# Kernel optimization log

Hardware: AMD Instinct MI355X
Metric: run time of the kernel (lower is better)

## Reference

```python
import jax, jax.numpy as jnp
import numpy as np

N, E = 50000, 800000
NFEAT, NHID, NHEADS, NCLASS = 512, 64, 8, 64
ALPHA = 0.2  # leaky relu negative slope


def setup_inputs() -> dict:
    key = jax.random.key(0)
    ks = jax.random.split(key, 8)
    x = jax.random.normal(ks[0], (N, NFEAT), jnp.float32)
    row = jax.random.randint(ks[1], (E,), 0, N)  # destination node i of each edge
    col = jax.random.randint(ks[2], (E,), 0, N)  # source node j of each edge
    W = jax.random.normal(ks[3], (NHEADS, NFEAT, NHID), jnp.float32) * (1.0 / np.sqrt(NFEAT))
    a = jax.random.normal(ks[4], (NHEADS, 2 * NHID), jnp.float32) * 0.1
    W_out = jax.random.normal(ks[5], (NHID * NHEADS, NCLASS), jnp.float32) * (1.0 / np.sqrt(NHID * NHEADS))
    a_out = jax.random.normal(ks[6], (2 * NCLASS,), jnp.float32) * 0.1
    return {"x": x, "row": row, "col": col, "W": W, "a": a, "W_out": W_out, "a_out": a_out}


def _gat_layer(h, W, a, row, col, n, alpha, concat):
    # h: [N, F_in], W: [F_in, F'], a: [2*F']
    Wh = h @ W                                   # [N, F']
    f = Wh.shape[-1]
    f_dst = Wh @ a[:f]                           # a^T part for target node i, [N]
    f_src = Wh @ a[f:]                           # a^T part for source node j, [N]
    e = jax.nn.leaky_relu(f_dst[row] + f_src[col], alpha)       # [E] attention logits
    # numerically stable segment softmax over incoming edges of each node
    m = jax.ops.segment_max(e, row, num_segments=n)
    m = jnp.where(jnp.isneginf(m), 0.0, m)       # nodes with no in-edges
    p = jnp.exp(e - m[row])
    denom = jax.ops.segment_sum(p, row, num_segments=n)
    att = p / jnp.maximum(denom[row], 1e-16)     # [E]
    out = jax.ops.segment_sum(att[:, None] * Wh[col], row, num_segments=n)  # [N, F']
    return jax.nn.elu(out) if concat else out


def reference(x, row, col, W, a, W_out, a_out):
    # eval mode: F.dropout is a no-op
    heads = [_gat_layer(x, W[h], a[h], row, col, N, ALPHA, True) for h in range(NHEADS)]
    h = jnp.concatenate(heads, axis=1)           # [N, NHID*NHEADS]
    return _gat_layer(h, W_out, a_out, row, col, N, ALPHA, False)  # [N, NCLASS]
```

## Files before the change

### kernel.cpp

```cpp
#include <hip/hip_runtime.h>
#include <cstdint>
#include <cstddef>

#define NN      50000
#define MPAD    50048
#define EE      800000
#define NHEADS  8
#define HID_TOT 512
#define NCLASS  64
#define ALPHA_LRELU 0.2f
#define NB1     196
#define CAP1    128
#define CAP2    128

typedef unsigned short u16;
typedef __attribute__((ext_vector_type(8))) unsigned short ushort8;
typedef __attribute__((ext_vector_type(4))) unsigned short ushort4v;

__device__ __forceinline__ float bf2f(u16 v) {
    return __uint_as_float(((unsigned)v) << 16);
}
__device__ __forceinline__ u16 f2bf(float f) {
    unsigned u = __float_as_uint(f);
    return (u16)((u + 0x7fffu + ((u >> 16) & 1u)) >> 16);
}

#define PREP_R0 (MPAD * 64)
#define PREP_R1 (512 * 512)
#define PREP_R2 (64 * 512)
#define PREP_R3 ((MPAD - NN) * 64)
#define PREP_TOT (PREP_R0 + PREP_R1 + PREP_R2 + PREP_R3)

__global__ __launch_bounds__(256) void prep_all(const float* __restrict__ x,
                                                const float* __restrict__ W,
                                                const float* __restrict__ W_out,
                                                u16* __restrict__ xb,
                                                u16* __restrict__ Wt1,
                                                u16* __restrict__ Wto,
                                                u16* __restrict__ h1b) {
    int g = blockIdx.x * 256 + threadIdx.x;
    if (g < PREP_R0) {
        int r = g >> 6;
        int c = (g & 63) * 8;
        ushort8 o = (ushort8)0;
        if (r < NN) {
            const float4 v0 = *(const float4*)(x + (size_t)r * 512 + c);
            const float4 v1 = *(const float4*)(x + (size_t)r * 512 + c + 4);
            o[0] = f2bf(v0.x); o[1] = f2bf(v0.y); o[2] = f2bf(v0.z); o[3] = f2bf(v0.w);
            o[4] = f2bf(v1.x); o[5] = f2bf(v1.y); o[6] = f2bf(v1.z); o[7] = f2bf(v1.w);
        }
        *(ushort8*)(xb + (size_t)r * 512 + c) = o;
        return;
    }
    g -= PREP_R0;
    if (g < PREP_R1) {
        int c = g >> 9, f = g & 511;
        int h = c >> 6, j = c & 63;
        Wt1[g] = f2bf(W[(h << 15) + (f << 6) + j]);
        return;
    }
    g -= PREP_R1;
    if (g < PREP_R2) {
        int n = g >> 9, k = g & 511;
        Wto[g] = f2bf(W_out[k * 64 + n]);
        return;
    }
    g -= PREP_R2;
    if (g < PREP_R3) {
        *(ushort8*)(h1b + (size_t)NN * 512 + (size_t)g * 8) = (ushort8)0;
    }
}


__global__ void fill_i32(int* __restrict__ p, int v, long n) {
    long i = (long)blockIdx.x * blockDim.x + threadIdx.x;
    if (i < n) p[i] = v;
}

__global__ void hist_rows(const int* __restrict__ row, int* __restrict__ cnt) {
    int e = blockIdx.x * 256 + threadIdx.x;
    if (e >= EE) return;
    atomicAdd(&cnt[row[e]], 1);
}

__global__ __launch_bounds__(256) void scan_blocksum(const int* __restrict__ cnt,
                                                     int* __restrict__ bsum) {
    int idx = blockIdx.x * 256 + threadIdx.x;
    int v = (idx < NN) ? cnt[idx] : 0;
    #pragma unroll
    for (int o = 32; o; o >>= 1) v += __shfl_xor(v, o);
    __shared__ int sw[4];
    int wave = threadIdx.x >> 6;
    if ((threadIdx.x & 63) == 0) sw[wave] = v;
    __syncthreads();
    if (threadIdx.x == 0) bsum[blockIdx.x] = sw[0] + sw[1] + sw[2] + sw[3];
}

__global__ __launch_bounds__(256) void scan_bsums(const int* __restrict__ bsum,
                                                  int* __restrict__ boff) {
    __shared__ int sh[256];
    int t = threadIdx.x;
    int v = (t < NB1) ? bsum[t] : 0;
    sh[t] = v;
    __syncthreads();
    for (int o = 1; o < 256; o <<= 1) {
        int cur = sh[t];
        int add = (t >= o) ? sh[t - o] : 0;
        __syncthreads();
        sh[t] = cur + add;
        __syncthreads();
    }
    if (t < NB1) boff[t] = sh[t] - v;
}

__global__ __launch_bounds__(256) void scan_write(const int* __restrict__ cnt,
                                                  const int* __restrict__ boff,
                                                  int* __restrict__ start,
                                                  int* __restrict__ wr) {
    __shared__ int sh[256];
    int t = threadIdx.x;
    int idx = blockIdx.x * 256 + t;
    int c = (idx < NN) ? cnt[idx] : 0;
    sh[t] = c;
    __syncthreads();
    for (int o = 1; o < 256; o <<= 1) {
        int cur = sh[t];
        int add = (t >= o) ? sh[t - o] : 0;
        __syncthreads();
        sh[t] = cur + add;
        __syncthreads();
    }
    if (idx < NN) {
        int excl = boff[blockIdx.x] + sh[t] - c;
        start[idx] = excl;
        wr[idx] = excl;
    }
    if (idx == 0) start[NN] = EE;
}

__global__ void scatter_edges(const int* __restrict__ row, const int* __restrict__ col,
                              int* __restrict__ wr, int* __restrict__ ecol) {
    int e = blockIdx.x * 256 + threadIdx.x;
    if (e >= EE) return;
    int i = row[e];
    int pos = atomicAdd(&wr[i], 1);
    ecol[pos] = col[e];
}


__device__ __forceinline__ void load_lds_128(const u16* g, u16* l) {
    __builtin_amdgcn_global_load_lds((const __attribute__((address_space(1))) void*)g,
                                     (__attribute__((address_space(3))) void*)l,
                                     16, 0, 0);
}

typedef __attribute__((ext_vector_type(8))) short frag8;
typedef __attribute__((ext_vector_type(4))) float f32x4;

template <int BN, int OUT_MODE, bool FUSE_DOTS>
__global__ __launch_bounds__(256) void gemm_bf16(const u16* __restrict__ A,
                                                 const u16* __restrict__ Bt,
                                                 void* __restrict__ Cv,
                                                 int M, int N, int K,
                                                 const float* __restrict__ av,
                                                 float* __restrict__ fd,
                                                 float* __restrict__ fs) {
    constexpr int BM = 128, BK = 32;
    constexpr int WN = BN / 2;
    constexpr int NT = WN / 16;
    __shared__ u16 As[BM * BK];
    __shared__ u16 Bs[BN * BK];
    const int tid = threadIdx.x;
    const int wave = tid >> 6, lane = tid & 63;
    const int wm = wave & 1, wn = wave >> 1;
    const int bm = blockIdx.y * BM, bn = blockIdx.x * BN;
    const int q = lane >> 4, lr = lane & 15;

    f32x4 acc[4][NT] = {};

    for (int k0 = 0; k0 < K; k0 += BK) {
        #pragma unroll
        for (int c = wave; c < (BM * BK) / 512; c += 4) {
            int f = c * 512 + lane * 8;
            int row = f >> 5, ck = f & 31;
            load_lds_128(A + (size_t)(bm + row) * K + k0 + ck, As + c * 512);
        }
        #pragma unroll
        for (int c = wave; c < (BN * BK) / 512; c += 4) {
            int f = c * 512 + lane * 8;
            int row = f >> 5, ck = f & 31;
            load_lds_128(Bt + (size_t)(bn + row) * K + k0 + ck, Bs + c * 512);
        }
        __syncthreads();
        frag8 af[4], bfr[NT];
        #pragma unroll
        for (int am = 0; am < 4; am++)
            af[am] = *(const frag8*)(As + (wm * 64 + am * 16 + lr) * 32 + q * 8);
        #pragma unroll
        for (int bt = 0; bt < NT; bt++)
            bfr[bt] = *(const frag8*)(Bs + (wn * WN + bt * 16 + lr) * 32 + q * 8);
        #pragma unroll
        for (int am = 0; am < 4; am++)
            #pragma unroll
            for (int bt = 0; bt < NT; bt++)
                acc[am][bt] = __builtin_amdgcn_mfma_f32_16x16x32_bf16(af[am], bfr[bt], acc[am][bt], 0, 0, 0);
        __syncthreads();
    }

    float adv[NT], adv2[NT];
    int hd = 0;
    if (FUSE_DOTS) {
        hd = blockIdx.x * 2 + wn;
        const float* ah = av + hd * 128;
        #pragma unroll
        for (int bt = 0; bt < NT; bt++) {
            adv[bt]  = ah[bt * 16 + lr];
            adv2[bt] = ah[64 + bt * 16 + lr];
        }
    }

    #pragma unroll
    for (int am = 0; am < 4; am++) {
        #pragma unroll
        for (int reg = 0; reg < 4; reg++) {
            int gr = bm + wm * 64 + am * 16 + q * 4 + reg;
            bool inb = gr < M;
            if (inb) {
                #pragma unroll
                for (int bt = 0; bt < NT; bt++) {
                    int gc = bn + wn * WN + bt * 16 + lr;
                    float v = acc[am][bt][reg];
                    if (OUT_MODE == 0) ((float*)Cv)[(size_t)gr * N + gc] = v;
                    else               ((u16*)Cv)[(size_t)gr * N + gc] = f2bf(v);
                }
            }
            if (FUSE_DOTS) {
                float sd = 0.f, ss = 0.f;
                #pragma unroll
                for (int bt = 0; bt < NT; bt++) {
                    float v = acc[am][bt][reg];
                    sd += v * adv[bt];
                    ss += v * adv2[bt];
                }
                #pragma unroll
                for (int o = 1; o < 16; o <<= 1) {
                    sd += __shfl_xor(sd, o);
                    ss += __shfl_xor(ss, o);
                }
                if (lr == 0 && inb) {
                    fd[gr * 8 + hd] = sd;
                    fs[gr * 8 + hd] = ss;
                }
            }
        }
    }
}


__global__ __launch_bounds__(256) void dots2(const u16* __restrict__ Wh2b, const float* __restrict__ a_out,
                                             float* __restrict__ fd, float* __restrict__ fs) {
    __shared__ float as[128];
    if (threadIdx.x < 128) as[threadIdx.x] = a_out[threadIdx.x];
    __syncthreads();
    int n = blockIdx.x * 256 + threadIdx.x;
    if (n >= NN) return;
    const u16* w = Wh2b + (size_t)n * NCLASS;
    float sd = 0.f, ss = 0.f;
    #pragma unroll
    for (int c = 0; c < 8; c++) {
        ushort8 v8 = *(const ushort8*)(w + c * 8);
        #pragma unroll
        for (int k = 0; k < 8; k++) {
            float v = bf2f(v8[k]);
            sd += v * as[c * 8 + k];
            ss += v * as[64 + c * 8 + k];
        }
    }
    fd[n] = sd;
    fs[n] = ss;
}

__global__ __launch_bounds__(256) void agg1_fused(const int* __restrict__ start,
                                                  const int* __restrict__ ecol,
                                                  const float* __restrict__ fd,
                                                  const float* __restrict__ fs,
                                                  const u16* __restrict__ Whb,
                                                  u16* __restrict__ h1b) {
    __shared__ float vc[4][CAP1 * 8];
    const int w = threadIdx.x >> 6;
    const int i = blockIdx.x * 4 + w;
    const int lane = threadIdx.x & 63;
    const int g = lane >> 3, h = lane & 7;
    const int st = start[i], en = start[i + 1];

    const float fdv1 = fd[i * 8 + h];
    float m = -__builtin_huge_valf();
    for (int t = st + g; t < en; t += 8) {
        int j = ecol[t];
        float v = fdv1 + fs[j * 8 + h];
        v = v > 0.f ? v : ALPHA_LRELU * v;
        int c = t - st;
        if (c < CAP1) vc[w][c * 8 + h] = v;
        m = fmaxf(m, v);
    }
    m = fmaxf(m, __shfl_xor(m, 8));
    m = fmaxf(m, __shfl_xor(m, 16));
    m = fmaxf(m, __shfl_xor(m, 32));
    __syncthreads();

    const int hh = lane >> 3;
    const float mh = __shfl(m, hh);
    const float fdv2 = fd[i * 8 + hh];
    float acc[8] = {};
    float den = 0.f;
    int t = st;
    for (; t + 2 <= en; t += 2) {
        int c0 = t - st, c1 = c0 + 1;
        int j0 = ecol[t], j1 = ecol[t + 1];
        float v0, v1;
        if (c1 < CAP1) {
            v0 = vc[w][c0 * 8 + hh];
            v1 = vc[w][c1 * 8 + hh];
        } else {
            v0 = fdv2 + fs[j0 * 8 + hh]; v0 = v0 > 0.f ? v0 : ALPHA_LRELU * v0;
            v1 = fdv2 + fs[j1 * 8 + hh]; v1 = v1 > 0.f ? v1 : ALPHA_LRELU * v1;
        }
        float p0 = __expf(v0 - mh);
        float p1 = __expf(v1 - mh);
        den += p0 + p1;
        ushort8 w0 = *(const ushort8*)(Whb + (size_t)j0 * HID_TOT + lane * 8);
        ushort8 w1 = *(const ushort8*)(Whb + (size_t)j1 * HID_TOT + lane * 8);
        #pragma unroll
        for (int k = 0; k < 8; k++) acc[k] += p0 * bf2f(w0[k]);
        #pragma unroll
        for (int k = 0; k < 8; k++) acc[k] += p1 * bf2f(w1[k]);
    }
    if (t < en) {
        int c = t - st;
        int j = ecol[t];
        float v;
        if (c < CAP1) v = vc[w][c * 8 + hh];
        else { v = fdv2 + fs[j * 8 + hh]; v = v > 0.f ? v : ALPHA_LRELU * v; }
        float p = __expf(v - mh);
        den += p;
        ushort8 wv = *(const ushort8*)(Whb + (size_t)j * HID_TOT + lane * 8);
        #pragma unroll
        for (int k = 0; k < 8; k++) acc[k] += p * bf2f(wv[k]);
    }
    float rden = 1.0f / fmaxf(den, 1e-16f);
    ushort8 o8;
    #pragma unroll
    for (int k = 0; k < 8; k++) {
        float v = acc[k] * rden;
        v = v > 0.f ? v : (__expf(v) - 1.0f);
        o8[k] = f2bf(v);
    }
    *(ushort8*)(h1b + (size_t)i * HID_TOT + lane * 8) = o8;
}

__global__ __launch_bounds__(256) void agg2_fused(const int* __restrict__ start,
                                                  const int* __restrict__ ecol,
                                                  const float* __restrict__ fd,
                                                  const float* __restrict__ fs,
                                                  const u16* __restrict__ Wh2b,
                                                  float* __restrict__ out) {
    __shared__ float vc[4][CAP2];
    const int w = threadIdx.x >> 6;
    const int i = blockIdx.x * 4 + w;
    const int lane = threadIdx.x & 63;
    const int st = start[i], en = start[i + 1];
    const float fdv = fd[i];

    float m = -__builtin_huge_valf();
    for (int t = st + lane; t < en; t += 64) {
        int j = ecol[t];
        float v = fdv + fs[j];
        v = v > 0.f ? v : ALPHA_LRELU * v;
        int c = t - st;
        if (c < CAP2) vc[w][c] = v;
        m = fmaxf(m, v);
    }
    #pragma unroll
    for (int o = 32; o; o >>= 1) m = fmaxf(m, __shfl_xor(m, o));
    __syncthreads();

    const int g = lane >> 4, r = lane & 15;
    float acc[4] = {};
    float den = 0.f;
    for (int t = st + g; t < en; t += 4) {
        int c = t - st;
        float v;
        if (c < CAP2) {
            v = vc[w][c];
        } else {
            int jj = ecol[t];
            v = fdv + fs[jj];
            v = v > 0.f ? v : ALPHA_LRELU * v;
        }
        float p = __expf(v - m);
        den += p;
        int j = ecol[t];
        ushort4v wv = *(const ushort4v*)(Wh2b + (size_t)j * NCLASS + r * 4);
        #pragma unroll
        for (int k = 0; k < 4; k++) acc[k] += p * bf2f(wv[k]);
    }
    #pragma unroll
    for (int o = 16; o <= 32; o <<= 1) {
        den += __shfl_xor(den, o);
        #pragma unroll
        for (int k = 0; k < 4; k++) acc[k] += __shfl_xor(acc[k], o);
    }
    if (g == 0) {
        float rden = 1.0f / fmaxf(den, 1e-16f);
        float4 o4;
        o4.x = acc[0] * rden; o4.y = acc[1] * rden;
        o4.z = acc[2] * rden; o4.w = acc[3] * rden;
        *(float4*)(out + (size_t)i * NCLASS + r * 4) = o4;
    }
}


static inline int cdiv_l(long a, long b) { return (int)((a + b - 1) / b); }

extern "C" void kernel_launch(void* const* d_in, const int* in_sizes, int n_in,
                              void* d_out, int out_size, void* d_ws, size_t ws_size,
                              hipStream_t stream) {
    const float* x     = (const float*)d_in[0];
    const int*   row   = (const int*)d_in[1];
    const int*   col   = (const int*)d_in[2];
    const float* W     = (const float*)d_in[3];
    const float* a     = (const float*)d_in[4];
    const float* W_out = (const float*)d_in[5];
    const float* a_out = (const float*)d_in[6];
    float* out = (float*)d_out;

    char* wsb = (char*)d_ws;
    size_t off = 0;
    auto alloc = [&](size_t bytes) { char* p = wsb + off; off += (bytes + 255) & ~(size_t)255; return p; };
    u16*   xb     = (u16*)  alloc((size_t)MPAD * 512 * 2);
    u16*   Wcat_t = (u16*)  alloc((size_t)512 * 512 * 2);
    u16*   Wot_t  = (u16*)  alloc((size_t)64 * 512 * 2);
    u16*   Whb1   = (u16*)  alloc((size_t)NN * 512 * 2);
    float* fd1    = (float*)alloc((size_t)NN * 8 * 4);
    float* fs1    = (float*)alloc((size_t)NN * 8 * 4);
    u16*   h1b    = (u16*)  alloc((size_t)MPAD * 512 * 2);
    u16*   Wh2b   = (u16*)  alloc((size_t)NN * 64 * 2);
    float* fd2    = (float*)alloc((size_t)NN * 4);
    float* fs2    = (float*)alloc((size_t)NN * 4);
    int*   cnt    = (int*)  alloc((size_t)NN * 4);
    int*   startp = (int*)  alloc(((size_t)NN + 1) * 4);
    int*   wr     = (int*)  alloc((size_t)NN * 4);
    int*   ecol   = (int*)  alloc((size_t)EE * 4);
    int*   bsum   = (int*)  alloc((size_t)NB1 * 4);
    int*   boff   = (int*)  alloc((size_t)NB1 * 4);

    fill_i32<<<cdiv_l(NN, 256), 256, 0, stream>>>(cnt, 0, (long)NN);
    hist_rows<<<cdiv_l(EE, 256), 256, 0, stream>>>(row, cnt);
    scan_blocksum<<<NB1, 256, 0, stream>>>(cnt, bsum);
    scan_bsums<<<1, 256, 0, stream>>>(bsum, boff);
    scan_write<<<NB1, 256, 0, stream>>>(cnt, boff, startp, wr);
    scatter_edges<<<cdiv_l(EE, 256), 256, 0, stream>>>(row, col, wr, ecol);

    prep_all<<<cdiv_l(PREP_TOT, 256), 256, 0, stream>>>(x, W, W_out, xb, Wcat_t, Wot_t, h1b);

    {
        dim3 grid(512 / 128, cdiv_l(MPAD, 128));
        gemm_bf16<128, 1, true><<<grid, 256, 0, stream>>>(xb, Wcat_t, Whb1, NN, 512, 512,
                                                          a, fd1, fs1);
    }
    agg1_fused<<<NN / 4, 256, 0, stream>>>(startp, ecol, fd1, fs1, Whb1, h1b);

    {
        dim3 grid(1, cdiv_l(MPAD, 128));
        gemm_bf16<64, 1, false><<<grid, 256, 0, stream>>>(h1b, Wot_t, Wh2b, NN, 64, 512,
                                                          nullptr, nullptr, nullptr);
    }
    dots2<<<cdiv_l(NN, 256), 256, 0, stream>>>(Wh2b, a_out, fd2, fs2);
    agg2_fused<<<NN / 4, 256, 0, stream>>>(startp, ecol, fd2, fs2, Wh2b, out);
}
```

Baseline: 493.3 us.

## Drop softmax max pass, fuse second-layer attention dots into GEMM epilogue

Both aggregation kernels now compute exp(logit) directly, without the per-node max-reduction pass and its LDS cache of logits. This removes a full extra sweep over each node's edges and the associated gathers. The separate dots2 kernel is folded into the second GEMM's epilogue via a shared-memory partial reduction across waves. The zeroing of the padded h1b rows is also dropped. Skipping the max shift risks overflow in exp for large logits, and the padded rows are now left uninitialised.

```diff
diff --git a/kernel.cpp b/kernel.cpp
--- a/kernel.cpp
+++ b/kernel.cpp
@@ -10,8 +10,6 @@
 #define NCLASS  64
 #define ALPHA_LRELU 0.2f
 #define NB1     196
-#define CAP1    128
-#define CAP2    128
 
 typedef unsigned short u16;
 typedef __attribute__((ext_vector_type(8))) unsigned short ushort8;
@@ -28,16 +26,14 @@
 #define PREP_R0 (MPAD * 64)
 #define PREP_R1 (512 * 512)
 #define PREP_R2 (64 * 512)
-#define PREP_R3 ((MPAD - NN) * 64)
-#define PREP_TOT (PREP_R0 + PREP_R1 + PREP_R2 + PREP_R3)
+#define PREP_TOT (PREP_R0 + PREP_R1 + PREP_R2)
 
 __global__ __launch_bounds__(256) void prep_all(const float* __restrict__ x,
                                                 const float* __restrict__ W,
                                                 const float* __restrict__ W_out,
                                                 u16* __restrict__ xb,
                                                 u16* __restrict__ Wt1,
-                                                u16* __restrict__ Wto,
-                                                u16* __restrict__ h1b) {
+                                                u16* __restrict__ Wto) {
     int g = blockIdx.x * 256 + threadIdx.x;
     if (g < PREP_R0) {
         int r = g >> 6;
@@ -63,11 +59,6 @@
     if (g < PREP_R2) {
         int n = g >> 9, k = g & 511;
         Wto[g] = f2bf(W_out[k * 64 + n]);
-        return;
-    }
-    g -= PREP_R2;
-    if (g < PREP_R3) {
-        *(ushort8*)(h1b + (size_t)NN * 512 + (size_t)g * 8) = (ushort8)0;
     }
 }
 
@@ -157,7 +148,7 @@
 typedef __attribute__((ext_vector_type(8))) short frag8;
 typedef __attribute__((ext_vector_type(4))) float f32x4;
 
-template <int BN, int OUT_MODE, bool FUSE_DOTS>
+template <int BN, int OUT_MODE, int FUSE>
 __global__ __launch_bounds__(256) void gemm_bf16(const u16* __restrict__ A,
                                                  const u16* __restrict__ Bt,
                                                  void* __restrict__ Cv,
@@ -170,6 +161,8 @@
     constexpr int NT = WN / 16;
     __shared__ u16 As[BM * BK];
     __shared__ u16 Bs[BN * BK];
+    __shared__ float pd[2][2][64];
+    __shared__ float ps[2][2][64];
     const int tid = threadIdx.x;
     const int wave = tid >> 6, lane = tid & 63;
     const int wm = wave & 1, wn = wave >> 1;
@@ -209,13 +202,20 @@
 
     float adv[NT], adv2[NT];
     int hd = 0;
-    if (FUSE_DOTS) {
+    if (FUSE == 1) {
         hd = blockIdx.x * 2 + wn;
         const float* ah = av + hd * 128;
         #pragma unroll
         for (int bt = 0; bt < NT; bt++) {
             adv[bt]  = ah[bt * 16 + lr];
             adv2[bt] = ah[64 + bt * 16 + lr];
+        }
+    }
+    if (FUSE == 2) {
+        #pragma unroll
+        for (int bt = 0; bt < NT; bt++) {
+            adv[bt]  = av[wn * WN + bt * 16 + lr];
+            adv2[bt] = av[64 + wn * WN + bt * 16 + lr];
         }
     }
 
@@ -234,7 +234,7 @@
                     else               ((u16*)Cv)[(size_t)gr * N + gc] = f2bf(v);
                 }
             }
-            if (FUSE_DOTS) {
+            if (FUSE != 0) {
                 float sd = 0.f, ss = 0.f;
                 #pragma unroll
                 for (int bt = 0; bt < NT; bt++) {
@@ -247,37 +247,32 @@
                     sd += __shfl_xor(sd, o);
                     ss += __shfl_xor(ss, o);
                 }
-                if (lr == 0 && inb) {
-                    fd[gr * 8 + hd] = sd;
-                    fs[gr * 8 + hd] = ss;
+                if (FUSE == 1) {
+                    if (lr == 0 && inb) {
+                        fd[gr * 8 + hd] = sd;
+                        fs[gr * 8 + hd] = ss;
+                    }
+                } else {
+                    if (lr == 0) {
+                        int rr = am * 16 + q * 4 + reg;
+                        pd[wm][wn][rr] = sd;
+                        ps[wm][wn][rr] = ss;
+                    }
                 }
             }
         }
     }
-}
-
-
-__global__ __launch_bounds__(256) void dots2(const u16* __restrict__ Wh2b, const float* __restrict__ a_out,
-                                             float* __restrict__ fd, float* __restrict__ fs) {
-    __shared__ float as[128];
-    if (threadIdx.x < 128) as[threadIdx.x] = a_out[threadIdx.x];
-    __syncthreads();
-    int n = blockIdx.x * 256 + threadIdx.x;
-    if (n >= NN) return;
-    const u16* w = Wh2b + (size_t)n * NCLASS;
-    float sd = 0.f, ss = 0.f;
-    #pragma unroll
-    for (int c = 0; c < 8; c++) {
-        ushort8 v8 = *(const ushort8*)(w + c * 8);
-        #pragma unroll
-        for (int k = 0; k < 8; k++) {
-            float v = bf2f(v8[k]);
-            sd += v * as[c * 8 + k];
-            ss += v * as[64 + c * 8 + k];
-        }
-    }
-    fd[n] = sd;
-    fs[n] = ss;
+    if (FUSE == 2) {
+        __syncthreads();
+        if (tid < 128) {
+            int wmm = tid >> 6, rr = tid & 63;
+            int gr = bm + wmm * 64 + rr;
+            if (gr < M) {
+                fd[gr] = pd[wmm][0][rr] + pd[wmm][1][rr];
+                fs[gr] = ps[wmm][0][rr] + ps[wmm][1][rr];
+            }
+        }
+    }
 }
 
 __global__ __launch_bounds__(256) void agg1_fused(const int* __restrict__ start,
@@ -286,62 +281,33 @@
                                                   const float* __restrict__ fs,
                                                   const u16* __restrict__ Whb,
                                                   u16* __restrict__ h1b) {
-    __shared__ float vc[4][CAP1 * 8];
-    const int w = threadIdx.x >> 6;
-    const int i = blockIdx.x * 4 + w;
+    const int i = blockIdx.x * 4 + (threadIdx.x >> 6);
     const int lane = threadIdx.x & 63;
-    const int g = lane >> 3, h = lane & 7;
+    const int hh = lane >> 3;
     const int st = start[i], en = start[i + 1];
-
-    const float fdv1 = fd[i * 8 + h];
-    float m = -__builtin_huge_valf();
-    for (int t = st + g; t < en; t += 8) {
-        int j = ecol[t];
-        float v = fdv1 + fs[j * 8 + h];
-        v = v > 0.f ? v : ALPHA_LRELU * v;
-        int c = t - st;
-        if (c < CAP1) vc[w][c * 8 + h] = v;
-        m = fmaxf(m, v);
-    }
-    m = fmaxf(m, __shfl_xor(m, 8));
-    m = fmaxf(m, __shfl_xor(m, 16));
-    m = fmaxf(m, __shfl_xor(m, 32));
-    __syncthreads();
-
-    const int hh = lane >> 3;
-    const float mh = __shfl(m, hh);
-    const float fdv2 = fd[i * 8 + hh];
+    const float fdv = fd[i * 8 + hh];
+
     float acc[8] = {};
     float den = 0.f;
     int t = st;
     for (; t + 2 <= en; t += 2) {
-        int c0 = t - st, c1 = c0 + 1;
         int j0 = ecol[t], j1 = ecol[t + 1];
-        float v0, v1;
-        if (c1 < CAP1) {
-            v0 = vc[w][c0 * 8 + hh];
-            v1 = vc[w][c1 * 8 + hh];
-        } else {
-            v0 = fdv2 + fs[j0 * 8 + hh]; v0 = v0 > 0.f ? v0 : ALPHA_LRELU * v0;
-            v1 = fdv2 + fs[j1 * 8 + hh]; v1 = v1 > 0.f ? v1 : ALPHA_LRELU * v1;
-        }
-        float p0 = __expf(v0 - mh);
-        float p1 = __expf(v1 - mh);
-        den += p0 + p1;
+        float v0 = fdv + fs[j0 * 8 + hh]; v0 = v0 > 0.f ? v0 : ALPHA_LRELU * v0;
+        float v1 = fdv + fs[j1 * 8 + hh]; v1 = v1 > 0.f ? v1 : ALPHA_LRELU * v1;
+        float p0 = __expf(v0);
+        float p1 = __expf(v1);
         ushort8 w0 = *(const ushort8*)(Whb + (size_t)j0 * HID_TOT + lane * 8);
         ushort8 w1 = *(const ushort8*)(Whb + (size_t)j1 * HID_TOT + lane * 8);
+        den += p0 + p1;
         #pragma unroll
         for (int k = 0; k < 8; k++) acc[k] += p0 * bf2f(w0[k]);
         #pragma unroll
         for (int k = 0; k < 8; k++) acc[k] += p1 * bf2f(w1[k]);
     }
     if (t < en) {
-        int c = t - st;
         int j = ecol[t];
-        float v;
-        if (c < CAP1) v = vc[w][c * 8 + hh];
-        else { v = fdv2 + fs[j * 8 + hh]; v = v > 0.f ? v : ALPHA_LRELU * v; }
-        float p = __expf(v - mh);
+        float v = fdv + fs[j * 8 + hh]; v = v > 0.f ? v : ALPHA_LRELU * v;
+        float p = __expf(v);
         den += p;
         ushort8 wv = *(const ushort8*)(Whb + (size_t)j * HID_TOT + lane * 8);
         #pragma unroll
@@ -364,42 +330,20 @@
                                                   const float* __restrict__ fs,
                                                   const u16* __restrict__ Wh2b,
                                                   float* __restrict__ out) {
-    __shared__ float vc[4][CAP2];
-    const int w = threadIdx.x >> 6;
-    const int i = blockIdx.x * 4 + w;
+    const int i = blockIdx.x * 4 + (threadIdx.x >> 6);
     const int lane = threadIdx.x & 63;
+    const int g = lane >> 4, r = lane & 15;
     const int st = start[i], en = start[i + 1];
     const float fdv = fd[i];
 
-    float m = -__builtin_huge_valf();
-    for (int t = st + lane; t < en; t += 64) {
+    float acc[4] = {};
+    float den = 0.f;
+    for (int t = st + g; t < en; t += 4) {
         int j = ecol[t];
         float v = fdv + fs[j];
         v = v > 0.f ? v : ALPHA_LRELU * v;
-        int c = t - st;
-        if (c < CAP2) vc[w][c] = v;
-        m = fmaxf(m, v);
-    }
-    #pragma unroll
-    for (int o = 32; o; o >>= 1) m = fmaxf(m, __shfl_xor(m, o));
-    __syncthreads();
-
-    const int g = lane >> 4, r = lane & 15;
-    float acc[4] = {};
-    float den = 0.f;
-    for (int t = st + g; t < en; t += 4) {
-        int c = t - st;
-        float v;
-        if (c < CAP2) {
-            v = vc[w][c];
-        } else {
-            int jj = ecol[t];
-            v = fdv + fs[jj];
-            v = v > 0.f ? v : ALPHA_LRELU * v;
-        }
-        float p = __expf(v - m);
+        float p = __expf(v);
         den += p;
-        int j = ecol[t];
         ushort4v wv = *(const ushort4v*)(Wh2b + (size_t)j * NCLASS + r * 4);
         #pragma unroll
         for (int k = 0; k < 4; k++) acc[k] += p * bf2f(wv[k]);
@@ -461,20 +405,19 @@
     scan_write<<<NB1, 256, 0, stream>>>(cnt, boff, startp, wr);
     scatter_edges<<<cdiv_l(EE, 256), 256, 0, stream>>>(row, col, wr, ecol);
 
-    prep_all<<<cdiv_l(PREP_TOT, 256), 256, 0, stream>>>(x, W, W_out, xb, Wcat_t, Wot_t, h1b);
+    prep_all<<<cdiv_l(PREP_TOT, 256), 256, 0, stream>>>(x, W, W_out, xb, Wcat_t, Wot_t);
 
     {
         dim3 grid(512 / 128, cdiv_l(MPAD, 128));
-        gemm_bf16<128, 1, true><<<grid, 256, 0, stream>>>(xb, Wcat_t, Whb1, NN, 512, 512,
-                                                          a, fd1, fs1);
+        gemm_bf16<128, 1, 1><<<grid, 256, 0, stream>>>(xb, Wcat_t, Whb1, NN, 512, 512,
+                                                       a, fd1, fs1);
     }
     agg1_fused<<<NN / 4, 256, 0, stream>>>(startp, ecol, fd1, fs1, Whb1, h1b);
 
     {
         dim3 grid(1, cdiv_l(MPAD, 128));
-        gemm_bf16<64, 1, false><<<grid, 256, 0, stream>>>(h1b, Wot_t, Wh2b, NN, 64, 512,
-                                                          nullptr, nullptr, nullptr);
-    }
-    dots2<<<cdiv_l(NN, 256), 256, 0, stream>>>(Wh2b, a_out, fd2, fs2);
+        gemm_bf16<64, 1, 2><<<grid, 256, 0, stream>>>(h1b, Wot_t, Wh2b, NN, 64, 512,
+                                                      a_out, fd2, fs2);
+    }
     agg2_fused<<<NN / 4, 256, 0, stream>>>(startp, ecol, fd2, fs2, Wh2b, out);
 }
```

Result: no change. 492.0 us (-0.3%).
